# Optimization experiments

Measured on AMD Instinct MI355X. Metric: run time of the kernel, lower is better.

Reference implementation:

```python
import jax, jax.numpy as jnp
import numpy as np

NB = 8      # n_blocks
DIM = 256   # model dim (= context_len in source)
DI = 512    # dim_inner = dim * expand(2)
DCONV = 4   # depthwise conv kernel
NS = 16     # d_state
DTR = 16    # dt_rank = ceil(dim/16)
NE = 4      # experts
INNER = 512 # MoE FFN inner = dim * multi(2)
L = 8192    # sequence length
HOR = 32    # horizon
EPS = 1e-3


def setup_inputs() -> dict:
    key = jax.random.key(0)
    ks = jax.random.split(key, 16)
    s = 0.02
    f = lambda k, shp: jax.random.normal(k, shp, jnp.float32) * s
    return {
        "x": jax.random.normal(ks[0], (DIM, L), jnp.float32),
        "lin_w": f(ks[1], (DIM, DIM)),                      # shared by self.linear and self.out (tied)
        "in_proj_w": f(ks[2], (NB, 2 * DI, DIM)),
        "conv_w": f(ks[3], (NB, DI, 1, DCONV)),             # depthwise conv, groups=DI
        "conv_b": f(ks[4], (NB, DI)),
        "x_proj_w": f(ks[5], (NB, DTR + 2 * NS, DI)),
        "dt_proj_w": f(ks[6], (NB, DI, DTR)),
        "dt_proj_b": f(ks[7], (NB, DI)),
        "A_log": jnp.tile(jnp.log(jnp.arange(1, NS + 1, dtype=jnp.float32)), (NB, DI, 1)),
        "D_param": jnp.ones((NB, DI), jnp.float32),
        "out_proj_w": f(ks[8], (NB, DIM, DI)),
        "gate_w": f(ks[9], (NB, NE, DIM)),
        "gproj_w": f(ks[10], (NB, NE, INNER, DIM)),
        "uproj_w": f(ks[11], (NB, NE, INNER, DIM)),
        "dproj_w": f(ks[12], (NB, NE, DIM, INNER)),
        "rms_a_w": jnp.ones((DIM,), jnp.float32),
        "rms_f_w": jnp.ones((DIM,), jnp.float32),
        "head_w1": f(ks[13], (DIM, DIM)),
        "head_w2": f(ks[14], (HOR, DIM)),
    }


def _rmsnorm(h, w):
    return w * (h * jax.lax.rsqrt(jnp.mean(h * h, axis=-1, keepdims=True) + EPS))


def _mamba(h, ipw, cw, cb, xpw, dtw, dtb, alog, dpar, opw):
    b = h.shape[0]
    xr = jnp.einsum('bld,od->bol', h, ipw)            # (b, 2*DI, l)
    xc, res = jnp.split(xr, 2, axis=1)                # each (b, DI, l)
    # causal depthwise conv (padding=DCONV-1, sliced to length l)
    xc = jax.lax.conv_general_dilated(xc, cw, (1,), [(DCONV - 1, 0)],
                                      feature_group_count=DI,
                                      dimension_numbers=('NCH', 'OIH', 'NCH'))
    xc = jax.nn.silu(xc + cb[None, :, None])
    A = -jnp.exp(alog)                                # (DI, NS)
    xdbl = jnp.einsum('bdl,kd->blk', xc, xpw)         # (b, l, DTR+2*NS)
    dr, B, C = xdbl[..., :DTR], xdbl[..., DTR:DTR + NS], xdbl[..., DTR + NS:]
    delta = jax.nn.softplus(jnp.einsum('blr,dr->bld', dr, dtw) + dtb)
    dA = jnp.exp(jnp.einsum('bld,dn->lbdn', delta, A))          # (l, b, DI, NS)
    dBu = jnp.einsum('bld,bln,bdl->lbdn', delta, B, xc)         # (l, b, DI, NS)
    Cl = jnp.transpose(C, (1, 0, 2))                             # (l, b, NS)
    def step(carry, inp):
        a, bu, c = inp
        carry = a * carry + bu
        return carry, jnp.einsum('bdn,bn->bd', carry, c)
    _, ys = jax.lax.scan(step, jnp.zeros((b, DI, NS), xc.dtype), (dA, dBu, Cl))
    y = jnp.transpose(ys, (1, 2, 0)) + xc * dpar[:, None]        # (b, DI, l)
    y = y * jax.nn.silu(res)
    return jnp.einsum('bdl,od->blo', y, opw)                     # (b, l, DIM)


def _moe(h, gw, gp, up, dp):
    shp = h.shape
    xf = h.reshape(-1, shp[-1])                       # (T, DIM)
    scores = xf @ gw.T                                # (T, NE)
    vals, idx = jax.lax.top_k(scores, 2)
    w = jax.nn.softmax(vals, axis=-1)                 # (T, 2)
    g = jax.nn.silu(jnp.einsum('td,ehd->teh', xf, gp))
    u = jnp.einsum('td,ehd->teh', xf, up)
    eo = jnp.einsum('teh,edh->ted', g * u, dp)        # (T, NE, DIM)
    we = jnp.sum(w[..., None] * jax.nn.one_hot(idx, NE, dtype=xf.dtype), axis=1)  # (T, NE)
    return jnp.einsum('te,ted->td', we, eo).reshape(shp)


def reference(x, lin_w, in_proj_w, conv_w, conv_b, x_proj_w, dt_proj_w, dt_proj_b,
              A_log, D_param, out_proj_w, gate_w, gproj_w, uproj_w, dproj_w,
              rms_a_w, rms_f_w, head_w1, head_w2):
    h = x.T[None]                                     # (1, L, DIM)
    h = h @ lin_w.T
    for i in range(NB):
        resi = h
        h = _rmsnorm(h, rms_a_w)
        h = _mamba(h, in_proj_w[i], conv_w[i], conv_b[i], x_proj_w[i],
                   dt_proj_w[i], dt_proj_b[i], A_log[i], D_param[i], out_proj_w[i])
        h = h + resi
        resi = h
        h = _moe(h, gate_w[i], gproj_w[i], uproj_w[i], dproj_w[i])
        h = _rmsnorm(h, rms_f_w)
        h = h + resi
    h = h @ lin_w.T                                   # self.out (tied weight)
    h = jax.nn.silu(h @ head_w1.T) @ head_w2.T        # head
    return jax.nn.sigmoid(h[0].T)                     # (HOR, L)
```

## Files before the change

### kernel.cpp

```cpp
#include <hip/hip_runtime.h>

typedef unsigned short u16;
typedef unsigned int u32;
using bf16x8 = __attribute__((ext_vector_type(8))) short;
using f32x4 = __attribute__((ext_vector_type(4))) float;

constexpr int kL = 8192;
constexpr int kDIM = 256;
constexpr int kDI = 512;
constexpr int kNB = 8;
constexpr float kEPS = 1e-3f;

__device__ __forceinline__ u16 f2b(float f) {
  u32 x = __builtin_bit_cast(u32, f);
  x += 0x7fffu + ((x >> 16) & 1u);
  return (u16)(x >> 16);
}
__device__ __forceinline__ float b2f(u16 u) {
  return __builtin_bit_cast(float, (u32)u << 16);
}
__device__ __forceinline__ float sigm(float x) { return 1.f / (1.f + __expf(-x)); }
__device__ __forceinline__ float softplus_fast(float x) {
  return fmaxf(x, 0.f) + __logf(1.f + __expf(-fabsf(x)));
}

__device__ __forceinline__ void async_cp16(const void* g, void* l) {
  __builtin_amdgcn_global_load_lds((const __attribute__((address_space(1))) u32*)g,
                                   (__attribute__((address_space(3))) u32*)l, 16, 0, 0);
}

struct Cvt2 {
  const float* s[23];
  u16* d[23];
  int n[23];
  int mode[23];
  int bstart[24];
  int nseg;
};
__global__ __launch_bounds__(256) void cvt2_k(Cvt2 dd) {
  const int b = blockIdx.x;
  int seg = 0;
  for (int i = 1; i < dd.nseg; ++i) seg += (b >= dd.bstart[i]) ? 1 : 0;
  const int lb = b - dd.bstart[seg];
  const float* s = dd.s[seg];
  u16* d = dd.d[seg];
  const int n = dd.n[seg];
  const int mode = dd.mode[seg];
  #pragma unroll
  for (int it = 0; it < 4; ++it) {
    const int e4 = lb * 1024 + it * 256 + threadIdx.x;
    const int i = e4 * 4;
    if (i >= n) break;
    const float4 v = ((const float4*)s)[e4];
    ushort4 o = make_ushort4(f2b(v.x), f2b(v.y), f2b(v.z), f2b(v.w));
    size_t dst;
    if (mode == 0) {
      dst = (size_t)i;
    } else if (mode == 1) {
      const int row = i >> 8, col = i & 255;
      const int drow = (row >> 9) * 1024 + ((row >> 4) & 31) * 32 + (row & 15);
      dst = (size_t)drow * 256 + col;
    } else {
      const int bb = i >> 19, e = (i >> 17) & 3, nr = (i >> 9) & 255, j = i & 511;
      dst = (size_t)bb * 524288 + (size_t)nr * 2048 + e * 512 + j;
    }
    *(ushort4*)&d[dst] = o;
  }
}

__global__ __launch_bounds__(256) void transpose_x_k(const float* __restrict__ x, u16* __restrict__ xT) {
  __shared__ float tile[32][33];
  int l0 = blockIdx.x * 32, d0 = blockIdx.y * 32;
  int tx = threadIdx.x, ty = threadIdx.y;
  #pragma unroll
  for (int i = 0; i < 32; i += 8)
    tile[ty + i][tx] = x[(size_t)(d0 + ty + i) * kL + l0 + tx];
  __syncthreads();
  #pragma unroll
  for (int i = 0; i < 32; i += 8)
    xT[(size_t)(l0 + ty + i) * kDIM + d0 + tx] = f2b(tile[tx][ty + i]);
}

template <int BM, int BN, int TR, int TC, int WCN, int MODE>
__global__ __launch_bounds__(256) void gemm_t(
    const u16* __restrict__ A, int lda,
    const u16* __restrict__ W, int ldw,
    void* __restrict__ C, int ldc,
    int N, int K, int pstride)
{
  constexpr int BNR = (BN + 63) & ~63;
  __shared__ u16 As[BM * 64];
  __shared__ u16 Bs[BNR * 64];
  const int tid = threadIdx.x;
  const int lane = tid & 63;
  const int wave = tid >> 6;
  const int bm = blockIdx.x * BM;
  const int bn = blockIdx.y * BN;
  const int wrow = (wave / WCN) * (TR * 16);
  const int wcol = (wave % WCN) * (TC * 16);
  const int kchunk = K / (int)gridDim.z;
  const int kbeg = blockIdx.z * kchunk;
  const int kend = kbeg + kchunk;

  f32x4 acc[TR][TC];
  #pragma unroll
  for (int r = 0; r < TR; ++r)
    #pragma unroll
    for (int c = 0; c < TC; ++c)
      acc[r][c] = f32x4{0.f, 0.f, 0.f, 0.f};

  for (int k0 = kbeg; k0 < kend; k0 += 64) {
    #pragma unroll
    for (int it = 0; it < BM * 64 / 2048; ++it) {
      int flat = (it * 256 + tid) * 8;
      int r = flat >> 6;
      int gc = ((((flat >> 3) & 7) ^ (r & 7)) << 3);
      async_cp16(A + (size_t)(bm + r) * lda + k0 + gc, &As[flat]);
    }
    #pragma unroll
    for (int it = 0; it < BNR * 64 / 2048; ++it) {
      int flat = (it * 256 + tid) * 8;
      int r = flat >> 6;
      int gc = ((((flat >> 3) & 7) ^ (r & 7)) << 3);
      int n = bn + r;
      if (n > N - 1) n = N - 1;
      async_cp16(W + (size_t)n * ldw + k0 + gc, &Bs[flat]);
    }
    __syncthreads();
    #pragma unroll
    for (int kk = 0; kk < 64; kk += 32) {
      const int kc = (kk >> 3) + (lane >> 4);
      const int mrow = lane & 15;
      bf16x8 a[TR], b[TC];
      #pragma unroll
      for (int rr = 0; rr < TR; ++rr) {
        int row = wrow + rr * 16 + mrow;
        a[rr] = *(const bf16x8*)&As[row * 64 + ((kc ^ (row & 7)) << 3)];
      }
      #pragma unroll
      for (int cc = 0; cc < TC; ++cc) {
        int row = wcol + cc * 16 + mrow;
        b[cc] = *(const bf16x8*)&Bs[row * 64 + ((kc ^ (row & 7)) << 3)];
      }
      #pragma unroll
      for (int rr = 0; rr < TR; ++rr)
        #pragma unroll
        for (int cc = 0; cc < TC; ++cc)
          acc[rr][cc] = __builtin_amdgcn_mfma_f32_16x16x32_bf16(a[rr], b[cc], acc[rr][cc], 0, 0, 0);
    }
    __syncthreads();
  }

  const int colb = bn + wcol + (lane & 15);
  const int rowb = bm + wrow + ((lane >> 4) << 2);
  #pragma unroll
  for (int rr = 0; rr < TR; ++rr)
    #pragma unroll
    for (int cc = 0; cc < TC; ++cc) {
      int col = colb + cc * 16;
      if (col >= N) continue;
      #pragma unroll
      for (int i = 0; i < 4; ++i) {
        const int row = rowb + rr * 16 + i;
        size_t off = (size_t)row * ldc + col;
        float v = acc[rr][cc][i];
        if constexpr (MODE == 0) ((float*)C)[off] = v;
        else if constexpr (MODE == 2) ((u16*)C)[off] = f2b(v);
        else if constexpr (MODE == 3) ((u16*)C)[off] = f2b(v * sigm(v));
        else if constexpr (MODE == 4) atomicAdd(&((float*)C)[off], v);
        else if constexpr (MODE == 5) ((float*)C)[off + (size_t)blockIdx.z * pstride] = v;
        else if constexpr (MODE == 7) ((float*)C)[(size_t)col * kL + row] = sigm(v);
      }
    }
}

__global__ __launch_bounds__(512, 1) void moe_mega_k(
    float* __restrict__ h, const float* __restrict__ hpart,
    const float* __restrict__ gw,
    const u16* __restrict__ Wgu, const u16* __restrict__ Wd,
    const float* __restrict__ wf, const float* __restrict__ wa,
    u16* __restrict__ hb2, u16* __restrict__ hn)
{
  __shared__ u16 Ah[32 * 256];
  __shared__ u16 Ts[32 * 512];
  __shared__ u16 Ws[2][256 * 64];
  __shared__ float WeS[32][4];
  const int tid = threadIdx.x;
  const int lane = tid & 63;
  const int quad = lane >> 4;
  const int m16 = lane & 15;
  const int wave = tid >> 6;
  const int wcol = wave * 32;
  const int r0 = blockIdx.x * 32;
  const int prow = tid >> 4;
  const int pcol = (tid & 15) * 16;

  float hv[16];
  {
    const size_t base = (size_t)(r0 + prow) * 256 + pcol;
    #pragma unroll
    for (int j = 0; j < 16; j += 4) {
      float4 v = *(const float4*)(h + base + j);
      #pragma unroll
      for (int z = 0; z < 4; ++z) {
        const float4 pv = *(const float4*)(hpart + (size_t)z * 2097152 + base + j);
        v.x += pv.x; v.y += pv.y; v.z += pv.z; v.w += pv.w;
      }
      hv[j] = v.x; hv[j + 1] = v.y; hv[j + 2] = v.z; hv[j + 3] = v.w;
    }
  }
  {
    float p[4];
    #pragma unroll
    for (int e = 0; e < 4; ++e) {
      float s = 0.f;
      #pragma unroll
      for (int j = 0; j < 16; ++j) s += hv[j] * gw[e * 256 + pcol + j];
      p[e] = s;
    }
    #pragma unroll
    for (int o = 8; o > 0; o >>= 1) {
      p[0] += __shfl_xor(p[0], o); p[1] += __shfl_xor(p[1], o);
      p[2] += __shfl_xor(p[2], o); p[3] += __shfl_xor(p[3], o);
    }
    if ((tid & 15) == 0) {
      int i0 = 0;
      #pragma unroll
      for (int e = 1; e < 4; ++e) if (p[e] > p[i0]) i0 = e;
      int i1 = -1;
      #pragma unroll
      for (int e = 0; e < 4; ++e) {
        if (e == i0) continue;
        if (i1 < 0 || p[e] > p[i1]) i1 = e;
      }
      const float tt = __expf(p[i1] - p[i0]);
      float o0 = 1.f / (1.f + tt), o1 = tt / (1.f + tt);
      WeS[prow][0] = 0.f; WeS[prow][1] = 0.f; WeS[prow][2] = 0.f; WeS[prow][3] = 0.f;
      WeS[prow][i0] = o0; WeS[prow][i1] = o1;
    }
    #pragma unroll
    for (int cc = 0; cc < 2; ++cc) {
      const int chunk = (pcol >> 3) + cc;
      const int sw = ((chunk ^ (prow & 7)) << 3);
      u16 tmp[8];
      #pragma unroll
      for (int j = 0; j < 8; ++j) tmp[j] = f2b(hv[cc * 8 + j]);
      *(bf16x8*)&Ah[prow * 256 + sw] = *(bf16x8*)tmp;
    }
  }
  __syncthreads();

  f32x4 macc[2][2];
  #pragma unroll
  for (int rt = 0; rt < 2; ++rt)
    #pragma unroll
    for (int ct = 0; ct < 2; ++ct) macc[rt][ct] = f32x4{0.f, 0.f, 0.f, 0.f};

  auto stage_gu = [&](int buf, int e, int nc, int k0) {
    #pragma unroll
    for (int it = 0; it < 4; ++it) {
      const int flat = (it * 512 + tid) * 8;
      const int r = flat >> 6;
      const int gc = ((((flat >> 3) & 7) ^ (r & 7)) << 3);
      async_cp16(Wgu + (size_t)(e * 1024 + nc * 256 + r) * 256 + k0 + gc, &Ws[buf][flat]);
    }
  };
  auto stage_dp = [&](int buf, int e, int k0) {
    #pragma unroll
    for (int it = 0; it < 4; ++it) {
      const int flat = (it * 512 + tid) * 8;
      const int r = flat >> 6;
      const int gc = ((((flat >> 3) & 7) ^ (r & 7)) << 3);
      async_cp16(Wd + (size_t)r * 2048 + e * 512 + k0 + gc, &Ws[buf][flat]);
    }
  };

  for (int e = 0; e < 4; ++e) {
    for (int nc = 0; nc < 4; ++nc) {
      f32x4 acc[2][2];
      #pragma unroll
      for (int rt = 0; rt < 2; ++rt)
        #pragma unroll
        for (int ct = 0; ct < 2; ++ct) acc[rt][ct] = f32x4{0.f, 0.f, 0.f, 0.f};
      stage_gu(0, e, nc, 0);
      __syncthreads();
      #pragma unroll
      for (int k0i = 0; k0i < 4; ++k0i) {
        if (k0i < 3) stage_gu((k0i + 1) & 1, e, nc, (k0i + 1) * 64);
        const u16* buf = Ws[k0i & 1];
        #pragma unroll
        for (int kk = 0; kk < 64; kk += 32) {
          const int kcs = (kk >> 3) + quad;
          bf16x8 a[2], b[2];
          #pragma unroll
          for (int rt = 0; rt < 2; ++rt) {
            const int row = rt * 16 + m16;
            const int ch = ((k0i * 64 + kk) >> 3) + quad;
            a[rt] = *(const bf16x8*)&Ah[row * 256 + ((ch ^ (row & 7)) << 3)];
          }
          #pragma unroll
          for (int ct = 0; ct < 2; ++ct) {
            const int n = wcol + ct * 16 + m16;
            b[ct] = *(const bf16x8*)&buf[n * 64 + ((kcs ^ (n & 7)) << 3)];
          }
          #pragma unroll
          for (int rt = 0; rt < 2; ++rt)
            #pragma unroll
            for (int ct = 0; ct < 2; ++ct)
              acc[rt][ct] = __builtin_amdgcn_mfma_f32_16x16x32_bf16(a[rt], b[ct], acc[rt][ct], 0, 0, 0);
        }
        __syncthreads();
      }
      const int group = nc * 8 + wave;
      const int j = group * 16 + m16;
      #pragma unroll
      for (int rt = 0; rt < 2; ++rt)
        #pragma unroll
        for (int i = 0; i < 4; ++i) {
          const int row = rt * 16 + quad * 4 + i;
          const float g = acc[rt][0][i];
          const float u = acc[rt][1][i];
          const float val = g * sigm(g) * u * WeS[row][e];
          Ts[row * 512 + (((j >> 3) ^ (row & 7)) << 3) + (j & 7)] = f2b(val);
        }
    }
    __syncthreads();
    stage_dp(0, e, 0);
    __syncthreads();
    #pragma unroll
    for (int k0i = 0; k0i < 8; ++k0i) {
      if (k0i < 7) stage_dp((k0i + 1) & 1, e, (k0i + 1) * 64);
      const u16* buf = Ws[k0i & 1];
      #pragma unroll
      for (int kk = 0; kk < 64; kk += 32) {
        const int kcs = (kk >> 3) + quad;
        bf16x8 a[2], b[2];
        #pragma unroll
        for (int rt = 0; rt < 2; ++rt) {
          const int row = rt * 16 + m16;
          const int ch = ((k0i * 64 + kk) >> 3) + quad;
          a[rt] = *(const bf16x8*)&Ts[row * 512 + ((ch ^ (row & 7)) << 3)];
        }
        #pragma unroll
        for (int ct = 0; ct < 2; ++ct) {
          const int n = wcol + ct * 16 + m16;
          b[ct] = *(const bf16x8*)&buf[n * 64 + ((kcs ^ (n & 7)) << 3)];
        }
        #pragma unroll
        for (int rt = 0; rt < 2; ++rt)
          #pragma unroll
          for (int ct = 0; ct < 2; ++ct)
            macc[rt][ct] = __builtin_amdgcn_mfma_f32_16x16x32_bf16(a[rt], b[ct], macc[rt][ct], 0, 0, 0);
      }
      __syncthreads();
    }
  }

  float* MoeS = (float*)Ts;
  __syncthreads();
  #pragma unroll
  for (int rt = 0; rt < 2; ++rt)
    #pragma unroll
    for (int ct = 0; ct < 2; ++ct)
      #pragma unroll
      for (int i = 0; i < 4; ++i)
        MoeS[(rt * 16 + quad * 4 + i) * 256 + wcol + ct * 16 + m16] = macc[rt][ct][i];
  __syncthreads();

  float mv[16];
  float ss = 0.f;
  #pragma unroll
  for (int j = 0; j < 16; ++j) {
    mv[j] = MoeS[prow * 256 + pcol + j];
    ss += mv[j] * mv[j];
  }
  #pragma unroll
  for (int o = 8; o > 0; o >>= 1) ss += __shfl_xor(ss, o);
  const float r1 = rsqrtf(ss * (1.f / 256.f) + kEPS);
  float ss2 = 0.f;
  #pragma unroll
  for (int j = 0; j < 16; ++j) {
    hv[j] += wf[pcol + j] * mv[j] * r1;
    ss2 += hv[j] * hv[j];
  }
  #pragma unroll
  for (int o = 8; o > 0; o >>= 1) ss2 += __shfl_xor(ss2, o);
  const float r2 = rsqrtf(ss2 * (1.f / 256.f) + kEPS);

  const size_t base = (size_t)(r0 + prow) * 256 + pcol;
  #pragma unroll
  for (int j = 0; j < 16; j += 4)
    *(float4*)(h + base + j) = float4{hv[j], hv[j + 1], hv[j + 2], hv[j + 3]};
  #pragma unroll
  for (int j = 0; j < 16; j += 4) {
    *(ushort4*)(hb2 + base + j) = make_ushort4(f2b(hv[j]), f2b(hv[j + 1]), f2b(hv[j + 2]), f2b(hv[j + 3]));
    *(ushort4*)(hn + base + j) = make_ushort4(
        f2b(wa[pcol + j] * hv[j] * r2), f2b(wa[pcol + j + 1] * hv[j + 1] * r2),
        f2b(wa[pcol + j + 2] * hv[j + 2] * r2), f2b(wa[pcol + j + 3] * hv[j + 3] * r2));
  }
}

__device__ __forceinline__ float block_sum256(float v) {
  #pragma unroll
  for (int o = 32; o > 0; o >>= 1) v += __shfl_down(v, o);
  __shared__ float red[4];
  __syncthreads();
  if ((threadIdx.x & 63) == 0) red[threadIdx.x >> 6] = v;
  __syncthreads();
  return red[0] + red[1] + red[2] + red[3];
}

__global__ __launch_bounds__(256) void rms_a_k(const float* __restrict__ h, const float* __restrict__ w,
                                               u16* __restrict__ hn) {
  const int l = blockIdx.x, t = threadIdx.x;
  const float v = h[(size_t)l * kDIM + t];
  const float ssum = block_sum256(v * v);
  const float r = rsqrtf(ssum * (1.f / 256.f) + kEPS);
  hn[(size_t)l * kDIM + t] = f2b(w[t] * v * r);
}

__global__ __launch_bounds__(256) void conv_silu_k(const u16* __restrict__ xz, const float* __restrict__ cw,
                                                   const float* __restrict__ cb,
                                                   u16* __restrict__ xcb, u16* __restrict__ zsb,
                                                   float* __restrict__ xdbl) {
  const int i4 = blockIdx.x * 256 + threadIdx.x;
  if (i4 < 98304) *(float4*)&xdbl[i4 * 4] = float4{0.f, 0.f, 0.f, 0.f};
  const int l = i4 >> 7;
  const int d = (i4 & 127) * 4;
  float acc[4];
  const float4 cbv = *(const float4*)&cb[d];
  acc[0] = cbv.x; acc[1] = cbv.y; acc[2] = cbv.z; acc[3] = cbv.w;
  #pragma unroll
  for (int j = 0; j < 4; ++j) {
    const int ll = l - 3 + j;
    if (ll >= 0) {
      const ushort4 xv = *(const ushort4*)&xz[(size_t)ll * 1024 + d];
      acc[0] += cw[(d + 0) * 4 + j] * b2f(xv.x);
      acc[1] += cw[(d + 1) * 4 + j] * b2f(xv.y);
      acc[2] += cw[(d + 2) * 4 + j] * b2f(xv.z);
      acc[3] += cw[(d + 3) * 4 + j] * b2f(xv.w);
    }
  }
  ushort4 xo, zo;
  const ushort4 zv = *(const ushort4*)&xz[(size_t)l * 1024 + 512 + d];
  float z0 = b2f(zv.x), z1 = b2f(zv.y), z2 = b2f(zv.z), z3 = b2f(zv.w);
  xo.x = f2b(acc[0] * sigm(acc[0])); xo.y = f2b(acc[1] * sigm(acc[1]));
  xo.z = f2b(acc[2] * sigm(acc[2])); xo.w = f2b(acc[3] * sigm(acc[3]));
  zo.x = f2b(z0 * sigm(z0)); zo.y = f2b(z1 * sigm(z1));
  zo.z = f2b(z2 * sigm(z2)); zo.w = f2b(z3 * sigm(z3));
  *(ushort4*)&xcb[(size_t)l * 512 + d] = xo;
  *(ushort4*)&zsb[(size_t)l * 512 + d] = zo;
}

__global__ __launch_bounds__(256) void scan_a_k(const float* __restrict__ xdbl, const u16* __restrict__ xcb,
                                                const float* __restrict__ A_log, const float* __restrict__ dtw,
                                                const float* __restrict__ dtb,
                                                u16* __restrict__ delta,
                                                float* __restrict__ aprod, float* __restrict__ bacc) {
  const int c = blockIdx.x;
  const int t = threadIdx.x;
  const int half = t & 1;
  const int d = blockIdx.y * 128 + (t >> 1);
  const int l0 = c * 64;
  __shared__ float Xs[64][32];
  for (int i = t; i < 2048; i += 256)
    Xs[i >> 5][i & 31] = xdbl[(size_t)(l0 + (i >> 5)) * 48 + (i & 31)];
  __syncthreads();
  float wd[8], Ad[8];
  #pragma unroll
  for (int j = 0; j < 8; ++j) wd[j] = dtw[d * 16 + half * 8 + j];
  const float bd = dtb[d];
  #pragma unroll
  for (int n = 0; n < 8; ++n) Ad[n] = -__expf(A_log[d * 16 + half * 8 + n]);
  float s[8], ap[8];
  #pragma unroll
  for (int n = 0; n < 8; ++n) { s[n] = 0.f; ap[n] = 1.f; }
  #pragma unroll 4
  for (int lr = 0; lr < 64; ++lr) {
    const float4 dr0 = *(const float4*)&Xs[lr][half * 8];
    const float4 dr1 = *(const float4*)&Xs[lr][half * 8 + 4];
    float p0 = dr0.x * wd[0] + dr0.y * wd[1] + dr0.z * wd[2] + dr0.w * wd[3];
    float p1 = dr1.x * wd[4] + dr1.y * wd[5] + dr1.z * wd[6] + dr1.w * wd[7];
    float dot = p0 + p1;
    dot += __shfl_xor(dot, 1);
    const float dl = softplus_fast(dot + bd);
    const int l = l0 + lr;
    if (!half) delta[(size_t)l * 512 + d] = f2b(dl);
    const float du = dl * b2f(xcb[(size_t)l * 512 + d]);
    const float4 B0 = *(const float4*)&Xs[lr][16 + half * 8];
    const float4 B1 = *(const float4*)&Xs[lr][16 + half * 8 + 4];
    const float Bv[8] = {B0.x, B0.y, B0.z, B0.w, B1.x, B1.y, B1.z, B1.w};
    #pragma unroll
    for (int n = 0; n < 8; ++n) {
      const float a = __expf(dl * Ad[n]);
      s[n] = fmaf(a, s[n], du * Bv[n]);
      ap[n] *= a;
    }
  }
  const int base = c * 8192 + d * 16 + half * 8;
  #pragma unroll
  for (int n = 0; n < 8; ++n) { aprod[base + n] = ap[n]; bacc[base + n] = s[n]; }
}

__global__ __launch_bounds__(256) void scan_b_k(const float* __restrict__ aprod, const float* __restrict__ bacc,
                                                float* __restrict__ sinit) {
  const int st = blockIdx.x * 256 + threadIdx.x;
  float cur = 0.f;
  float a0 = aprod[st], b0 = bacc[st];
  for (int c = 0; c < 128; ++c) {
    float a1 = 0.f, b1 = 0.f;
    if (c + 1 < 128) {
      a1 = aprod[(size_t)(c + 1) * 8192 + st];
      b1 = bacc[(size_t)(c + 1) * 8192 + st];
    }
    sinit[(size_t)c * 8192 + st] = cur;
    cur = fmaf(a0, cur, b0);
    a0 = a1; b0 = b1;
  }
}

__global__ __launch_bounds__(256) void scan_c_k(const float* __restrict__ xdbl, const u16* __restrict__ xcb,
                                                const u16* __restrict__ zsb, const float* __restrict__ A_log,
                                                const u16* __restrict__ delta,
                                                const float* __restrict__ sinit,
                                                const float* __restrict__ Dp, u16* __restrict__ yv) {
  const int c = blockIdx.x;
  const int t = threadIdx.x;
  const int half = t & 1;
  const int d = blockIdx.y * 128 + (t >> 1);
  const int l0 = c * 64;
  __shared__ float Xs[64][32];
  for (int i = t; i < 2048; i += 256)
    Xs[i >> 5][i & 31] = xdbl[(size_t)(l0 + (i >> 5)) * 48 + 16 + (i & 31)];
  __syncthreads();
  float Ad[8];
  #pragma unroll
  for (int n = 0; n < 8; ++n) Ad[n] = -__expf(A_log[d * 16 + half * 8 + n]);
  float s[8];
  const int base = c * 8192 + d * 16 + half * 8;
  #pragma unroll
  for (int n = 0; n < 8; ++n) s[n] = sinit[base + n];
  const float Dd = Dp[d];
  #pragma unroll 4
  for (int lr = 0; lr < 64; ++lr) {
    const int l = l0 + lr;
    const float dl = b2f(delta[(size_t)l * 512 + d]);
    const float xv = b2f(xcb[(size_t)l * 512 + d]);
    const float zs = b2f(zsb[(size_t)l * 512 + d]);
    const float du = dl * xv;
    const float4 B0 = *(const float4*)&Xs[lr][half * 8];
    const float4 B1 = *(const float4*)&Xs[lr][half * 8 + 4];
    const float4 C0 = *(const float4*)&Xs[lr][16 + half * 8];
    const float4 C1 = *(const float4*)&Xs[lr][16 + half * 8 + 4];
    const float Bv[8] = {B0.x, B0.y, B0.z, B0.w, B1.x, B1.y, B1.z, B1.w};
    const float Cv[8] = {C0.x, C0.y, C0.z, C0.w, C1.x, C1.y, C1.z, C1.w};
    float y = 0.f;
    #pragma unroll
    for (int n = 0; n < 8; ++n) {
      const float a = __expf(dl * Ad[n]);
      s[n] = fmaf(a, s[n], du * Bv[n]);
      y = fmaf(s[n], Cv[n], y);
    }
    y += __shfl_xor(y, 1);
    if (!half) yv[(size_t)l * 512 + d] = f2b((y + xv * Dd) * zs);
  }
}

extern "C" void kernel_launch(void* const* d_in, const int* in_sizes, int n_in,
                              void* d_out, int out_size, void* d_ws, size_t ws_size,
                              hipStream_t stream) {
  const float* x        = (const float*)d_in[0];
  const float* lin_w    = (const float*)d_in[1];
  const float* in_proj  = (const float*)d_in[2];
  const float* conv_w   = (const float*)d_in[3];
  const float* conv_b   = (const float*)d_in[4];
  const float* x_proj   = (const float*)d_in[5];
  const float* dt_w     = (const float*)d_in[6];
  const float* dt_b     = (const float*)d_in[7];
  const float* A_log    = (const float*)d_in[8];
  const float* D_param  = (const float*)d_in[9];
  const float* out_proj = (const float*)d_in[10];
  const float* gate_w   = (const float*)d_in[11];
  const float* gproj    = (const float*)d_in[12];
  const float* uproj    = (const float*)d_in[13];
  const float* dproj    = (const float*)d_in[14];
  const float* rms_a_w  = (const float*)d_in[15];
  const float* rms_f_w  = (const float*)d_in[16];
  const float* head_w1  = (const float*)d_in[17];
  const float* head_w2  = (const float*)d_in[18];

  char* p = (char*)d_ws;
  auto alloc = [&](size_t bytes) -> char* {
    char* r = p;
    p += (bytes + 255) & ~(size_t)255;
    return r;
  };

  u16* lin_b  = (u16*)alloc(65536 * 2);
  u16* ipw_b  = (u16*)alloc((size_t)2097152 * 2);
  u16* xpw_b  = (u16*)alloc((size_t)196608 * 2);
  u16* opw_b  = (u16*)alloc((size_t)1048576 * 2);
  u16* gupw_b = (u16*)alloc((size_t)8388608 * 2);
  u16* dpw_b  = (u16*)alloc((size_t)4194304 * 2);
  u16* hw1_b  = (u16*)alloc(65536 * 2);
  u16* hw2_b  = (u16*)alloc(8192 * 2);

  u16* xT     = (u16*)alloc((size_t)kL * kDIM * 2);
  float* h    = (float*)alloc((size_t)kL * kDIM * 4);
  u16* hn     = (u16*)alloc((size_t)kL * kDIM * 2);
  u16* hb2    = (u16*)alloc((size_t)kL * kDIM * 2);
  float* xdbl = (float*)alloc((size_t)kL * 48 * 4);
  u16* fb     = (u16*)alloc((size_t)kL * kDIM * 2);
  u16* h2b    = (u16*)alloc((size_t)kL * kDIM * 2);
  u16* xz     = (u16*)alloc((size_t)kL * 1024 * 2);
  u16* xcb    = (u16*)alloc((size_t)kL * kDI * 2);
  u16* zsb    = (u16*)alloc((size_t)kL * kDI * 2);
  u16* yv     = (u16*)alloc((size_t)kL * kDI * 2);
  u16* delta  = (u16*)alloc((size_t)kL * kDI * 2);
  float* aprod = (float*)alloc((size_t)128 * 8192 * 4);
  float* bacc  = (float*)alloc((size_t)128 * 8192 * 4);
  float* sinit = (float*)alloc((size_t)128 * 8192 * 4);
  float* hpart = (float*)alloc((size_t)4 * kL * kDIM * 4);

  if ((size_t)(p - (char*)d_ws) > ws_size) return;

  Cvt2 dd;
  int seg = 0, blk = 0;
  auto add = [&](const float* s, u16* d, int n, int mode) {
    dd.s[seg] = s; dd.d[seg] = d; dd.n[seg] = n; dd.mode[seg] = mode;
    dd.bstart[seg] = blk;
    blk += (n + 4095) / 4096;
    ++seg;
  };
  add(lin_w, lin_b, 65536, 0);
  add(in_proj, ipw_b, 2097152, 0);
  add(x_proj, xpw_b, 196608, 0);
  add(out_proj, opw_b, 1048576, 0);
  add(head_w1, hw1_b, 65536, 0);
  add(head_w2, hw2_b, 8192, 0);
  for (int i = 0; i < kNB; ++i) {
    add(gproj + (size_t)i * 524288, gupw_b + (size_t)i * 1048576, 524288, 1);
    add(uproj + (size_t)i * 524288, gupw_b + (size_t)i * 1048576 + 4096, 524288, 1);
  }
  add(dproj, dpw_b, 4194304, 2);
  dd.nseg = seg;
  dd.bstart[seg] = blk;
  cvt2_k<<<blk, 256, 0, stream>>>(dd);
  transpose_x_k<<<dim3(kL / 32, kDIM / 32), dim3(32, 8), 0, stream>>>(x, xT);

  gemm_t<64, 128, 2, 4, 2, 0><<<dim3(128, 2, 1), 256, 0, stream>>>(
      xT, 256, lin_b, 256, h, 256, 256, 256, 0);
  rms_a_k<<<kL, 256, 0, stream>>>(h, rms_a_w, hn);

  for (int i = 0; i < kNB; ++i) {
    gemm_t<128, 128, 4, 4, 2, 2><<<dim3(64, 8, 1), 256, 0, stream>>>(
        hn, 256, ipw_b + (size_t)i * 262144, 256, xz, 1024, 1024, 256, 0);
    conv_silu_k<<<kL * kDI / 1024, 256, 0, stream>>>(xz, conv_w + (size_t)i * 2048,
                                                     conv_b + (size_t)i * 512, xcb, zsb, xdbl);
    gemm_t<128, 48, 2, 3, 1, 4><<<dim3(64, 1, 8), 256, 0, stream>>>(
        xcb, 512, xpw_b + (size_t)i * 24576, 512, xdbl, 48, 48, 512, 0);
    scan_a_k<<<dim3(128, 4), 256, 0, stream>>>(xdbl, xcb, A_log + (size_t)i * 8192,
                                               dt_w + (size_t)i * 8192, dt_b + (size_t)i * 512,
                                               delta, aprod, bacc);
    scan_b_k<<<32, 256, 0, stream>>>(aprod, bacc, sinit);
    scan_c_k<<<dim3(128, 4), 256, 0, stream>>>(xdbl, xcb, zsb, A_log + (size_t)i * 8192,
                                               delta, sinit, D_param + (size_t)i * 512, yv);
    gemm_t<128, 128, 4, 4, 2, 5><<<dim3(64, 2, 4), 256, 0, stream>>>(
        yv, 512, opw_b + (size_t)i * 131072, 512, hpart, 256, 256, 512, 2097152);
    moe_mega_k<<<256, 512, 0, stream>>>(h, hpart, gate_w + (size_t)i * 1024,
                                        gupw_b + (size_t)i * 1048576, dpw_b + (size_t)i * 524288,
                                        rms_f_w, rms_a_w, hb2, hn);
  }

  gemm_t<64, 128, 2, 4, 2, 2><<<dim3(128, 2, 1), 256, 0, stream>>>(
      hb2, 256, lin_b, 256, h2b, 256, 256, 256, 0);
  gemm_t<64, 128, 2, 4, 2, 3><<<dim3(128, 2, 1), 256, 0, stream>>>(
      h2b, 256, hw1_b, 256, fb, 256, 256, 256, 0);
  gemm_t<64, 128, 2, 4, 2, 7><<<dim3(128, 1, 1), 256, 0, stream>>>(
      fb, 256, hw2_b, 256, (float*)d_out, 32, 32, 256, 0);
}
```

Measured before the change: 2.147 ms.

## Parallelize chunk-state scan, halve out_proj split-K, precompute GEMM load pointers

The serial 128-step inter-chunk scan (32 blocks) becomes a three-phase hierarchical scan: group reduce, a 16-step scan, then group propagate. This exposes much more parallelism, at the cost of two extra launches and extra memory traffic. The out_proj GEMM's split-K drops from 4 to 2, so there are fewer partial buffers to write and for the MoE kernel to re-read. The GEMM inner loop now uses precomputed, incrementing source pointers instead of recomputing addresses every iteration.

```diff
diff --git a/kernel.cpp b/kernel.cpp
--- a/kernel.cpp
+++ b/kernel.cpp
@@ -89,6 +89,8 @@
     int N, int K, int pstride)
 {
   constexpr int BNR = (BN + 63) & ~63;
+  constexpr int NA = BM * 64 / 2048;
+  constexpr int NBt = BNR * 64 / 2048;
   __shared__ u16 As[BM * 64];
   __shared__ u16 Bs[BNR * 64];
   const int tid = threadIdx.x;
@@ -100,7 +102,30 @@
   const int wcol = (wave % WCN) * (TC * 16);
   const int kchunk = K / (int)gridDim.z;
   const int kbeg = blockIdx.z * kchunk;
-  const int kend = kbeg + kchunk;
+  const int niter = kchunk >> 6;
+
+  const u16* aSrc[NA];
+  int aDst[NA];
+  #pragma unroll
+  for (int it = 0; it < NA; ++it) {
+    const int flat = (it * 256 + tid) * 8;
+    const int r = flat >> 6;
+    const int gc = ((((flat >> 3) & 7) ^ (r & 7)) << 3);
+    aDst[it] = flat;
+    aSrc[it] = A + (size_t)(bm + r) * lda + kbeg + gc;
+  }
+  const u16* bSrc[NBt];
+  int bDst[NBt];
+  #pragma unroll
+  for (int it = 0; it < NBt; ++it) {
+    const int flat = (it * 256 + tid) * 8;
+    const int r = flat >> 6;
+    const int gc = ((((flat >> 3) & 7) ^ (r & 7)) << 3);
+    int n = bn + r;
+    if (n > N - 1) n = N - 1;
+    bDst[it] = flat;
+    bSrc[it] = W + (size_t)n * ldw + kbeg + gc;
+  }
 
   f32x4 acc[TR][TC];
   #pragma unroll
@@ -109,22 +134,16 @@
     for (int c = 0; c < TC; ++c)
       acc[r][c] = f32x4{0.f, 0.f, 0.f, 0.f};
 
-  for (int k0 = kbeg; k0 < kend; k0 += 64) {
-    #pragma unroll
-    for (int it = 0; it < BM * 64 / 2048; ++it) {
-      int flat = (it * 256 + tid) * 8;
-      int r = flat >> 6;
-      int gc = ((((flat >> 3) & 7) ^ (r & 7)) << 3);
-      async_cp16(A + (size_t)(bm + r) * lda + k0 + gc, &As[flat]);
-    }
-    #pragma unroll
-    for (int it = 0; it < BNR * 64 / 2048; ++it) {
-      int flat = (it * 256 + tid) * 8;
-      int r = flat >> 6;
-      int gc = ((((flat >> 3) & 7) ^ (r & 7)) << 3);
-      int n = bn + r;
-      if (n > N - 1) n = N - 1;
-      async_cp16(W + (size_t)n * ldw + k0 + gc, &Bs[flat]);
+  for (int ki = 0; ki < niter; ++ki) {
+    #pragma unroll
+    for (int it = 0; it < NA; ++it) {
+      async_cp16(aSrc[it], &As[aDst[it]]);
+      aSrc[it] += 64;
+    }
+    #pragma unroll
+    for (int it = 0; it < NBt; ++it) {
+      async_cp16(bSrc[it], &Bs[bDst[it]]);
+      bSrc[it] += 64;
     }
     __syncthreads();
     #pragma unroll
@@ -202,7 +221,7 @@
     for (int j = 0; j < 16; j += 4) {
       float4 v = *(const float4*)(h + base + j);
       #pragma unroll
-      for (int z = 0; z < 4; ++z) {
+      for (int z = 0; z < 2; ++z) {
         const float4 pv = *(const float4*)(hpart + (size_t)z * 2097152 + base + j);
         v.x += pv.x; v.y += pv.y; v.z += pv.z; v.w += pv.w;
       }
@@ -502,20 +521,43 @@
   for (int n = 0; n < 8; ++n) { aprod[base + n] = ap[n]; bacc[base + n] = s[n]; }
 }
 
-__global__ __launch_bounds__(256) void scan_b_k(const float* __restrict__ aprod, const float* __restrict__ bacc,
-                                                float* __restrict__ sinit) {
+__global__ __launch_bounds__(256) void scan_b1_k(const float* __restrict__ aprod, const float* __restrict__ bacc,
+                                                 float* __restrict__ gp, float* __restrict__ gb) {
+  const int idx = blockIdx.x * 256 + threadIdx.x;
+  const int st = idx & 8191, g = idx >> 13;
+  float P = 1.f, S = 0.f;
+  #pragma unroll
+  for (int k = 0; k < 8; ++k) {
+    const int c = g * 8 + k;
+    const float a = aprod[(size_t)c * 8192 + st];
+    S = fmaf(a, S, bacc[(size_t)c * 8192 + st]);
+    P *= a;
+  }
+  gp[(size_t)g * 8192 + st] = P;
+  gb[(size_t)g * 8192 + st] = S;
+}
+
+__global__ __launch_bounds__(256) void scan_b2_k(const float* __restrict__ gp, const float* __restrict__ gb,
+                                                 float* __restrict__ ginit) {
   const int st = blockIdx.x * 256 + threadIdx.x;
   float cur = 0.f;
-  float a0 = aprod[st], b0 = bacc[st];
-  for (int c = 0; c < 128; ++c) {
-    float a1 = 0.f, b1 = 0.f;
-    if (c + 1 < 128) {
-      a1 = aprod[(size_t)(c + 1) * 8192 + st];
-      b1 = bacc[(size_t)(c + 1) * 8192 + st];
-    }
+  #pragma unroll
+  for (int g = 0; g < 16; ++g) {
+    ginit[(size_t)g * 8192 + st] = cur;
+    cur = fmaf(gp[(size_t)g * 8192 + st], cur, gb[(size_t)g * 8192 + st]);
+  }
+}
+
+__global__ __launch_bounds__(256) void scan_b3_k(const float* __restrict__ aprod, const float* __restrict__ bacc,
+                                                 const float* __restrict__ ginit, float* __restrict__ sinit) {
+  const int idx = blockIdx.x * 256 + threadIdx.x;
+  const int st = idx & 8191, g = idx >> 13;
+  float cur = ginit[(size_t)g * 8192 + st];
+  #pragma unroll
+  for (int k = 0; k < 8; ++k) {
+    const int c = g * 8 + k;
     sinit[(size_t)c * 8192 + st] = cur;
-    cur = fmaf(a0, cur, b0);
-    a0 = a1; b0 = b1;
+    cur = fmaf(aprod[(size_t)c * 8192 + st], cur, bacc[(size_t)c * 8192 + st]);
   }
 }
 
@@ -620,7 +662,10 @@
   float* aprod = (float*)alloc((size_t)128 * 8192 * 4);
   float* bacc  = (float*)alloc((size_t)128 * 8192 * 4);
   float* sinit = (float*)alloc((size_t)128 * 8192 * 4);
-  float* hpart = (float*)alloc((size_t)4 * kL * kDIM * 4);
+  float* gp    = (float*)alloc((size_t)16 * 8192 * 4);
+  float* gb    = (float*)alloc((size_t)16 * 8192 * 4);
+  float* ginit = (float*)alloc((size_t)16 * 8192 * 4);
+  float* hpart = (float*)alloc((size_t)2 * kL * kDIM * 4);
 
   if ((size_t)(p - (char*)d_ws) > ws_size) return;
 
@@ -662,10 +707,12 @@
     scan_a_k<<<dim3(128, 4), 256, 0, stream>>>(xdbl, xcb, A_log + (size_t)i * 8192,
                                                dt_w + (size_t)i * 8192, dt_b + (size_t)i * 512,
                                                delta, aprod, bacc);
-    scan_b_k<<<32, 256, 0, stream>>>(aprod, bacc, sinit);
+    scan_b1_k<<<512, 256, 0, stream>>>(aprod, bacc, gp, gb);
+    scan_b2_k<<<32, 256, 0, stream>>>(gp, gb, ginit);
+    scan_b3_k<<<512, 256, 0, stream>>>(aprod, bacc, ginit, sinit);
     scan_c_k<<<dim3(128, 4), 256, 0, stream>>>(xdbl, xcb, zsb, A_log + (size_t)i * 8192,
                                                delta, sinit, D_param + (size_t)i * 512, yv);
-    gemm_t<128, 128, 4, 4, 2, 5><<<dim3(64, 2, 4), 256, 0, stream>>>(
+    gemm_t<128, 128, 4, 4, 2, 5><<<dim3(64, 2, 2), 256, 0, stream>>>(
         yv, 512, opw_b + (size_t)i * 131072, 512, hpart, 256, 256, 512, 2097152);
     moe_mega_k<<<256, 512, 0, stream>>>(h, hpart, gate_w + (size_t)i * 1024,
                                         gupw_b + (size_t)i * 1048576, dpw_b + (size_t)i * 524288,
```

After: 2.008 ms. 6.5% less time.
